# Kernel optimization log

Measured on AMD Instinct MI355X. Metric: run time of the kernel, lower is better.

The kernel has to match this reference:

```python
import jax, jax.numpy as jnp
import numpy as np

DIM = 1024
NUM_HEADS = 16
HEAD_DIM = DIM // NUM_HEADS
B, L = 4, 4096


def setup_inputs() -> dict:
    key = jax.random.key(0)
    ks = jax.random.split(key, 11)
    s = 1.0 / np.sqrt(DIM)
    inp = {
        'q_seq': jax.random.normal(ks[0], (B, L, DIM), jnp.float32),
        'k_seq': jax.random.normal(ks[1], (B, L, DIM), jnp.float32),
        'v_seq': jax.random.normal(ks[2], (B, L, DIM), jnp.float32),
        'Wq': jax.random.normal(ks[3], (DIM, DIM), jnp.float32) * s,
        'bq': jax.random.normal(ks[4], (DIM,), jnp.float32) * s,
        'Wk': jax.random.normal(ks[5], (DIM, DIM), jnp.float32) * s,
        'bk': jax.random.normal(ks[6], (DIM,), jnp.float32) * s,
        'Wv': jax.random.normal(ks[7], (DIM, DIM), jnp.float32) * s,
        'bv': jax.random.normal(ks[8], (DIM,), jnp.float32) * s,
        'Wo': jax.random.normal(ks[9], (DIM, DIM), jnp.float32) * s,
        'bo': jax.random.normal(ks[10], (DIM,), jnp.float32) * s,
        'extract_common': 1,
    }
    return inp


def _heads(x):
    # [B, L, DIM] -> [B, H, L, D]
    Bb, Ll, _ = x.shape
    return x.reshape(Bb, Ll, NUM_HEADS, HEAD_DIM).transpose(0, 2, 1, 3)


def reference(q_seq, k_seq, v_seq, Wq, bq, Wk, bk, Wv, bv, Wo, bo, extract_common):
    Q = _heads(q_seq @ Wq.T + bq)   # [B, H, Lq, D]
    K = _heads(k_seq @ Wk.T + bk)   # [B, H, Lk, D]
    V = _heads(v_seq @ Wv.T + bv)   # [B, H, Lv, D]
    # softmax over the sequence dimension of K (torch dim=2 of [B,H,L,D])
    K_probs = jax.nn.softmax(K, axis=2)
    # context = K_probs^T @ V : [B, H, D, D]
    context = jnp.einsum('bhld,bhle->bhde', K_probs, V)
    attended = jnp.einsum('bhld,bhde->bhle', Q, context)  # [B, H, Lq, D]
    if extract_common:
        target = attended
    else:
        target = V - attended
    Bb, _, Ll, _ = target.shape
    target = target.transpose(0, 2, 1, 3).reshape(Bb, Ll, DIM)
    return target @ Wo.T + bo
```

## Files before the change

kernel.cpp:

```cpp
#include <hip/hip_runtime.h>
#include <cmath>

typedef __bf16 bf16x8 __attribute__((ext_vector_type(8)));
typedef float f32x4 __attribute__((ext_vector_type(4)));
typedef unsigned short us8 __attribute__((ext_vector_type(8)));

__device__ __forceinline__ unsigned short f2bf(float f) {
    union { float f; unsigned u; } x; x.f = f;
    unsigned u = x.u + 0x7FFFu + ((x.u >> 16) & 1u);
    return (unsigned short)(u >> 16);
}
__device__ __forceinline__ float bf2f(unsigned short h) {
    union { unsigned u; float f; } x; x.u = ((unsigned)h) << 16;
    return x.f;
}

__device__ __forceinline__ us8 cvt8(const float* p) {
    f32x4 a = *(const f32x4*)p;
    f32x4 b = *(const f32x4*)(p + 4);
    union { bf16x8 h; us8 u; } cv;
    cv.h[0] = (__bf16)a[0]; cv.h[1] = (__bf16)a[1];
    cv.h[2] = (__bf16)a[2]; cv.h[3] = (__bf16)a[3];
    cv.h[4] = (__bf16)b[0]; cv.h[5] = (__bf16)b[1];
    cv.h[6] = (__bf16)b[2]; cv.h[7] = (__bf16)b[3];
    return cv.u;
}

__device__ __forceinline__ void gl2lds16(const unsigned short* g, unsigned short* l) {
    __builtin_amdgcn_global_load_lds(
        (const __attribute__((address_space(1))) unsigned int*)g,
        (__attribute__((address_space(3))) unsigned int*)l, 16, 0, 0);
}

__global__ __launch_bounds__(256)
void cvt_kernel(const float* __restrict__ src, unsigned short* __restrict__ dst) {
    const size_t i = ((size_t)blockIdx.x * 256 + threadIdx.x) * 8;
    *(us8*)(dst + i) = cvt8(src + i);
}

__global__ __launch_bounds__(256)
void cvt_w4(const float* __restrict__ s0, const float* __restrict__ s1,
            const float* __restrict__ s2, const float* __restrict__ s3,
            unsigned short* __restrict__ d0, unsigned short* __restrict__ d1,
            unsigned short* __restrict__ d2, unsigned short* __restrict__ d3) {
    const float* sp[4] = {s0, s1, s2, s3};
    unsigned short* dp[4] = {d0, d1, d2, d3};
    const float* src = sp[blockIdx.y];
    unsigned short* dst = dp[blockIdx.y];
    const size_t i = ((size_t)blockIdx.x * 256 + threadIdx.x) * 8;
    *(us8*)(dst + i) = cvt8(src + i);
}

__device__ __forceinline__ void swz_tiles(int& m0, int& n0) {
    const int slot = blockIdx.x + (blockIdx.y << 3);
    const int w = ((slot & 7) << 7) | (slot >> 3);
    m0 = (w >> 3) << 7;
    n0 = (w & 7) << 7;
}

template<int MODE, bool BF>
__global__ __launch_bounds__(256)
void gemm_proj(const void* __restrict__ Ap, const void* __restrict__ Wp,
               const float* __restrict__ bias,
               unsigned short* __restrict__ outT,
               float* __restrict__ S)
{
    __shared__ __align__(16) unsigned short lds[17408];

    const int tid = threadIdx.x;
    const int wid = tid >> 6, lane = tid & 63;
    const int quad = lane >> 4, l16 = lane & 15;
    const int waveM = wid >> 1, waveN = wid & 1;
    int m0, n0; swz_tiles(m0, n0);
    const int srow = tid >> 2;
    const int scol = (tid & 3) * 8;
    const int r4 = lane >> 2, c8 = (lane & 3) * 8;

    f32x4 acc[4][4] = {};

    if (BF) {
        const unsigned short* A = (const unsigned short*)Ap;
        const unsigned short* W = (const unsigned short*)Wp;
        for (int s = wid; s < 8; s += 4) {
            const int row = s * 16 + r4;
            gl2lds16(A + (size_t)(m0 + row) * 1024 + c8, lds + s * 512);
            gl2lds16(W + (size_t)(n0 + row) * 1024 + c8, lds + 4096 + s * 512);
        }
    } else {
        const float* A = (const float*)Ap;
        const float* W = (const float*)Wp;
#pragma unroll
        for (int p = 0; p < 2; ++p) {
            const int row = p * 64 + srow;
            *(us8*)(lds + row * 32 + scol) = cvt8(A + (size_t)(m0 + row) * 1024 + scol);
            *(us8*)(lds + 4096 + row * 32 + scol) = cvt8(W + (size_t)(n0 + row) * 1024 + scol);
        }
    }
    __syncthreads();

    int cur = 0;
    for (int k0 = 0; k0 < 1024; k0 += 32) {
        const int nxt = cur ^ 1;
        if (k0 < 992) {
            if (BF) {
                const unsigned short* A = (const unsigned short*)Ap;
                const unsigned short* W = (const unsigned short*)Wp;
                for (int s = wid; s < 8; s += 4) {
                    const int row = s * 16 + r4;
                    gl2lds16(A + (size_t)(m0 + row) * 1024 + k0 + 32 + c8,
                             lds + nxt * 8192 + s * 512);
                    gl2lds16(W + (size_t)(n0 + row) * 1024 + k0 + 32 + c8,
                             lds + nxt * 8192 + 4096 + s * 512);
                }
            } else {
                const float* A = (const float*)Ap;
                const float* W = (const float*)Wp;
#pragma unroll
                for (int p = 0; p < 2; ++p) {
                    const int row = p * 64 + srow;
                    *(us8*)(lds + nxt * 8192 + row * 32 + scol) =
                        cvt8(A + (size_t)(m0 + row) * 1024 + k0 + 32 + scol);
                    *(us8*)(lds + nxt * 8192 + 4096 + row * 32 + scol) =
                        cvt8(W + (size_t)(n0 + row) * 1024 + k0 + 32 + scol);
                }
            }
        }
        const unsigned short* ldsA = lds + cur * 8192;
        const unsigned short* ldsB = ldsA + 4096;
        bf16x8 af[4], bfr[4];
#pragma unroll
        for (int i = 0; i < 4; ++i)
            af[i] = *(const bf16x8*)(ldsA + (waveM * 64 + i * 16 + l16) * 32 + quad * 8);
#pragma unroll
        for (int j = 0; j < 4; ++j)
            bfr[j] = *(const bf16x8*)(ldsB + (waveN * 64 + j * 16 + l16) * 32 + quad * 8);
#pragma unroll
        for (int i = 0; i < 4; ++i)
#pragma unroll
            for (int j = 0; j < 4; ++j)
                acc[i][j] = __builtin_amdgcn_mfma_f32_16x16x32_bf16(af[i], bfr[j], acc[i][j], 0, 0, 0);
        __syncthreads();
        cur = nxt;
    }

    const int b = m0 >> 12, l0 = m0 & 4095;
#pragma unroll
    for (int j = 0; j < 4; ++j) {
        const int nn = waveN * 64 + j * 16 + l16;
        const float bc = bias[n0 + nn];
        float ssum = 0.f;
#pragma unroll
        for (int i = 0; i < 4; ++i)
#pragma unroll
            for (int r = 0; r < 4; ++r) {
                const int mm = waveM * 64 + i * 16 + quad * 4 + r;
                float v = acc[i][j][r] + bc;
                if (MODE == 1) v = expf(fminf(fmaxf(v, -30.f), 30.f));
                lds[nn * 136 + mm] = f2bf(v);
                ssum += v;
            }
        if (MODE == 1) {
            ssum += __shfl_xor(ssum, 16);
            ssum += __shfl_xor(ssum, 32);
            if (lane < 16)
                atomicAdd(&S[(size_t)b * 1024 + n0 + waveN * 64 + j * 16 + lane], ssum);
        }
    }
    __syncthreads();
    const int seg = (tid & 15) * 8;
#pragma unroll
    for (int it = 0; it < 8; ++it) {
        const int nn = (tid >> 4) + it * 16;
        us8 v = *(const us8*)&lds[nn * 136 + seg];
        *(us8*)(outT + ((size_t)b * 1024 + n0 + nn) * 4096 + l0 + seg) = v;
    }
}

__global__ __launch_bounds__(256)
void ctx_kernel(const unsigned short* __restrict__ Vt,
                const unsigned short* __restrict__ Et,
                float* __restrict__ ctxf)
{
    __shared__ __align__(16) unsigned short lds[8192];

    const int tid = threadIdx.x;
    const int wid = tid >> 6, lane = tid & 63;
    const int quad = lane >> 4, l16 = lane & 15;
    const int b = blockIdx.z, h = blockIdx.y;
    const int lbase = blockIdx.x * 512;

    const unsigned short* Arow = Vt + ((size_t)b * 1024 + h * 64) * 4096;
    const unsigned short* Brow = Et + ((size_t)b * 1024 + h * 64) * 4096;

    const int srow = tid >> 2;
    const int scol = (tid & 3) * 8;

    f32x4 acc[4] = {};

    {
        us8 va = *(const us8*)(Arow + (size_t)srow * 4096 + lbase + scol);
        us8 vb = *(const us8*)(Brow + (size_t)srow * 4096 + lbase + scol);
        *(us8*)(lds + srow * 32 + scol) = va;
        *(us8*)(lds + 2048 + srow * 32 + scol) = vb;
    }
    __syncthreads();

    int cur = 0;
    for (int k0 = 0; k0 < 512; k0 += 32) {
        const int nxt = cur ^ 1;
        us8 na = {}, nb = {};
        const bool pf = (k0 < 480);
        if (pf) {
            na = *(const us8*)(Arow + (size_t)srow * 4096 + lbase + k0 + 32 + scol);
            nb = *(const us8*)(Brow + (size_t)srow * 4096 + lbase + k0 + 32 + scol);
        }
        const unsigned short* ldsA = lds + cur * 4096;
        const unsigned short* ldsB = ldsA + 2048;
        bf16x8 a = *(const bf16x8*)(ldsA + (wid * 16 + l16) * 32 + quad * 8);
#pragma unroll
        for (int j = 0; j < 4; ++j) {
            bf16x8 bb = *(const bf16x8*)(ldsB + (j * 16 + l16) * 32 + quad * 8);
            acc[j] = __builtin_amdgcn_mfma_f32_16x16x32_bf16(a, bb, acc[j], 0, 0, 0);
        }
        if (pf) {
            *(us8*)(lds + nxt * 4096 + srow * 32 + scol) = na;
            *(us8*)(lds + nxt * 4096 + 2048 + srow * 32 + scol) = nb;
        }
        __syncthreads();
        cur = nxt;
    }
    float* base = ctxf + ((size_t)(b * 16 + h)) * 4096;
#pragma unroll
    for (int j = 0; j < 4; ++j)
#pragma unroll
        for (int r = 0; r < 4; ++r) {
            const int e = wid * 16 + quad * 4 + r;
            const int d = j * 16 + l16;
            atomicAdd(base + e * 64 + d, acc[j][r]);
        }
}

__global__ __launch_bounds__(256)
void ctx_norm(const float* __restrict__ ctxf, const float* __restrict__ S,
              unsigned short* __restrict__ ctxb)
{
    const int i = blockIdx.x * 256 + threadIdx.x;
    const int d = i & 63;
    const int bh = i >> 12;
    const int b = bh >> 4, h = bh & 15;
    ctxb[i] = f2bf(ctxf[i] / S[b * 1024 + h * 64 + d]);
}

template<bool BF>
__global__ __launch_bounds__(256)
void gemm_qattn(const void* __restrict__ Ap, const void* __restrict__ Wp,
                const float* __restrict__ bias,
                const unsigned short* __restrict__ ctxb,
                const unsigned short* __restrict__ Vt,
                const int* __restrict__ ec,
                unsigned short* __restrict__ att)
{
    __shared__ __align__(16) unsigned short lds[26624];
    unsigned short* ldsQ = lds;
    unsigned short* ldsC = lds + 17408;

    const int tid = threadIdx.x;
    const int wid = tid >> 6, lane = tid & 63;
    const int quad = lane >> 4, l16 = lane & 15;
    const int waveM = wid >> 1, waveN = wid & 1;
    int m0, n0; swz_tiles(m0, n0);
    const int b = m0 >> 12;
    const int srow = tid >> 2, scol = (tid & 3) * 8;
    const int r4 = lane >> 2, c8 = (lane & 3) * 8;

    {
        const int e2 = tid >> 1;
        const int sg = (tid & 1) * 32;
        const unsigned short* src = ctxb +
            (((size_t)(b * 16) + (n0 >> 6) + (e2 >> 6)) * 64 + (e2 & 63)) * 64 + sg;
#pragma unroll
        for (int u = 0; u < 4; ++u)
            *(us8*)&ldsC[e2 * 72 + sg + u * 8] = *(const us8*)(src + u * 8);
    }

    f32x4 acc[4][4] = {};

    if (BF) {
        const unsigned short* A = (const unsigned short*)Ap;
        const unsigned short* W = (const unsigned short*)Wp;
        for (int s = wid; s < 8; s += 4) {
            const int row = s * 16 + r4;
            gl2lds16(A + (size_t)(m0 + row) * 1024 + c8, lds + s * 512);
            gl2lds16(W + (size_t)(n0 + row) * 1024 + c8, lds + 4096 + s * 512);
        }
    } else {
        const float* A = (const float*)Ap;
        const float* W = (const float*)Wp;
#pragma unroll
        for (int p = 0; p < 2; ++p) {
            const int row = p * 64 + srow;
            *(us8*)(lds + row * 32 + scol) = cvt8(A + (size_t)(m0 + row) * 1024 + scol);
            *(us8*)(lds + 4096 + row * 32 + scol) = cvt8(W + (size_t)(n0 + row) * 1024 + scol);
        }
    }
    __syncthreads();

    int cur = 0;
    for (int k0 = 0; k0 < 1024; k0 += 32) {
        const int nxt = cur ^ 1;
        if (k0 < 992) {
            if (BF) {
                const unsigned short* A = (const unsigned short*)Ap;
                const unsigned short* W = (const unsigned short*)Wp;
                for (int s = wid; s < 8; s += 4) {
                    const int row = s * 16 + r4;
                    gl2lds16(A + (size_t)(m0 + row) * 1024 + k0 + 32 + c8,
                             lds + nxt * 8192 + s * 512);
                    gl2lds16(W + (size_t)(n0 + row) * 1024 + k0 + 32 + c8,
                             lds + nxt * 8192 + 4096 + s * 512);
                }
            } else {
                const float* A = (const float*)Ap;
                const float* W = (const float*)Wp;
#pragma unroll
                for (int p = 0; p < 2; ++p) {
                    const int row = p * 64 + srow;
                    *(us8*)(lds + nxt * 8192 + row * 32 + scol) =
                        cvt8(A + (size_t)(m0 + row) * 1024 + k0 + 32 + scol);
                    *(us8*)(lds + nxt * 8192 + 4096 + row * 32 + scol) =
                        cvt8(W + (size_t)(n0 + row) * 1024 + k0 + 32 + scol);
                }
            }
        }
        const unsigned short* ldsA = lds + cur * 8192;
        const unsigned short* ldsB = ldsA + 4096;
        bf16x8 af[4], bfr[4];
#pragma unroll
        for (int i = 0; i < 4; ++i)
            af[i] = *(const bf16x8*)(ldsA + (waveM * 64 + i * 16 + l16) * 32 + quad * 8);
#pragma unroll
        for (int j = 0; j < 4; ++j)
            bfr[j] = *(const bf16x8*)(ldsB + (waveN * 64 + j * 16 + l16) * 32 + quad * 8);
#pragma unroll
        for (int i = 0; i < 4; ++i)
#pragma unroll
            for (int j = 0; j < 4; ++j)
                acc[i][j] = __builtin_amdgcn_mfma_f32_16x16x32_bf16(af[i], bfr[j], acc[i][j], 0, 0, 0);
        __syncthreads();
        cur = nxt;
    }

#pragma unroll
    for (int j = 0; j < 4; ++j) {
        const int nn = waveN * 64 + j * 16 + l16;
        const float bc = bias[n0 + nn];
#pragma unroll
        for (int i = 0; i < 4; ++i)
#pragma unroll
            for (int r = 0; r < 4; ++r) {
                const int mm = waveM * 64 + i * 16 + quad * 4 + r;
                ldsQ[mm * 136 + nn] = f2bf(acc[i][j][r] + bc);
            }
    }
    __syncthreads();

    f32x4 acc2[4][4] = {};
#pragma unroll
    for (int ks = 0; ks < 64; ks += 32) {
        bf16x8 aq[4], cq[4];
#pragma unroll
        for (int i = 0; i < 4; ++i)
            aq[i] = *(const bf16x8*)&ldsQ[(waveM * 64 + i * 16 + l16) * 136 + waveN * 64 + ks + quad * 8];
#pragma unroll
        for (int j = 0; j < 4; ++j)
            cq[j] = *(const bf16x8*)&ldsC[(waveN * 64 + j * 16 + l16) * 72 + ks + quad * 8];
#pragma unroll
        for (int i = 0; i < 4; ++i)
#pragma unroll
            for (int j = 0; j < 4; ++j)
                acc2[i][j] = __builtin_amdgcn_mfma_f32_16x16x32_bf16(aq[i], cq[j], acc2[i][j], 0, 0, 0);
    }

    const int common = ec[0];
#pragma unroll
    for (int i = 0; i < 4; ++i)
#pragma unroll
        for (int j = 0; j < 4; ++j)
#pragma unroll
            for (int r = 0; r < 4; ++r) {
                const int lrow = m0 + waveM * 64 + i * 16 + quad * 4 + r;
                const int chan = n0 + waveN * 64 + j * 16 + l16;
                float vv = acc2[i][j][r];
                if (!common)
                    vv = bf2f(Vt[((size_t)(lrow >> 12) * 1024 + chan) * 4096 + (lrow & 4095)]) - vv;
                att[(size_t)lrow * 1024 + chan] = f2bf(vv);
            }
}

template<bool BF>
__global__ __launch_bounds__(256)
void gemm_out(const unsigned short* __restrict__ A, const void* __restrict__ Wp,
              const float* __restrict__ bias,
              float* __restrict__ outP)
{
    __shared__ __align__(16) unsigned short lds[16384];

    const int tid = threadIdx.x;
    const int wid = tid >> 6, lane = tid & 63;
    const int quad = lane >> 4, l16 = lane & 15;
    const int waveM = wid >> 1, waveN = wid & 1;
    int m0, n0; swz_tiles(m0, n0);
    const int srow = tid >> 2, scol = (tid & 3) * 8;
    const int r4 = lane >> 2, c8 = (lane & 3) * 8;

    f32x4 acc[4][4] = {};

    if (BF) {
        const unsigned short* W = (const unsigned short*)Wp;
        for (int s = wid; s < 8; s += 4) {
            const int row = s * 16 + r4;
            gl2lds16(A + (size_t)(m0 + row) * 1024 + c8, lds + s * 512);
            gl2lds16(W + (size_t)(n0 + row) * 1024 + c8, lds + 4096 + s * 512);
        }
    } else {
        const float* W = (const float*)Wp;
#pragma unroll
        for (int p = 0; p < 2; ++p) {
            const int row = p * 64 + srow;
            *(us8*)(lds + row * 32 + scol) = *(const us8*)(A + (size_t)(m0 + row) * 1024 + scol);
            *(us8*)(lds + 4096 + row * 32 + scol) = cvt8(W + (size_t)(n0 + row) * 1024 + scol);
        }
    }
    __syncthreads();

    int cur = 0;
    for (int k0 = 0; k0 < 1024; k0 += 32) {
        const int nxt = cur ^ 1;
        if (k0 < 992) {
            if (BF) {
                const unsigned short* W = (const unsigned short*)Wp;
                for (int s = wid; s < 8; s += 4) {
                    const int row = s * 16 + r4;
                    gl2lds16(A + (size_t)(m0 + row) * 1024 + k0 + 32 + c8,
                             lds + nxt * 8192 + s * 512);
                    gl2lds16(W + (size_t)(n0 + row) * 1024 + k0 + 32 + c8,
                             lds + nxt * 8192 + 4096 + s * 512);
                }
            } else {
                const float* W = (const float*)Wp;
#pragma unroll
                for (int p = 0; p < 2; ++p) {
                    const int row = p * 64 + srow;
                    *(us8*)(lds + nxt * 8192 + row * 32 + scol) =
                        *(const us8*)(A + (size_t)(m0 + row) * 1024 + k0 + 32 + scol);
                    *(us8*)(lds + nxt * 8192 + 4096 + row * 32 + scol) =
                        cvt8(W + (size_t)(n0 + row) * 1024 + k0 + 32 + scol);
                }
            }
        }
        const unsigned short* ldsA = lds + cur * 8192;
        const unsigned short* ldsB = ldsA + 4096;
        bf16x8 af[4], bfr[4];
#pragma unroll
        for (int i = 0; i < 4; ++i)
            af[i] = *(const bf16x8*)(ldsA + (waveM * 64 + i * 16 + l16) * 32 + quad * 8);
#pragma unroll
        for (int j = 0; j < 4; ++j)
            bfr[j] = *(const bf16x8*)(ldsB + (waveN * 64 + j * 16 + l16) * 32 + quad * 8);
#pragma unroll
        for (int i = 0; i < 4; ++i)
#pragma unroll
            for (int j = 0; j < 4; ++j)
                acc[i][j] = __builtin_amdgcn_mfma_f32_16x16x32_bf16(af[i], bfr[j], acc[i][j], 0, 0, 0);
        __syncthreads();
        cur = nxt;
    }

#pragma unroll
    for (int j = 0; j < 4; ++j) {
        const int col = n0 + waveN * 64 + j * 16 + l16;
        const float bc = bias[col];
#pragma unroll
        for (int i = 0; i < 4; ++i)
#pragma unroll
            for (int r = 0; r < 4; ++r) {
                const int row = m0 + waveM * 64 + i * 16 + quad * 4 + r;
                outP[(size_t)row * 1024 + col] = acc[i][j][r] + bc;
            }
    }
}

extern "C" void kernel_launch(void* const* d_in, const int* in_sizes, int n_in,
                              void* d_out, int out_size, void* d_ws, size_t ws_size,
                              hipStream_t stream)
{
    const float* q  = (const float*)d_in[0];
    const float* k  = (const float*)d_in[1];
    const float* v  = (const float*)d_in[2];
    const float* Wq = (const float*)d_in[3];
    const float* bq = (const float*)d_in[4];
    const float* Wk = (const float*)d_in[5];
    const float* bk = (const float*)d_in[6];
    const float* Wv = (const float*)d_in[7];
    const float* bv = (const float*)d_in[8];
    const float* Wo = (const float*)d_in[9];
    const float* bo = (const float*)d_in[10];
    const int* ec   = (const int*)d_in[11];

    char* ws = (char*)d_ws;
    const size_t NEED_FAST = 110641152;
    const dim3 gblk(8, 128, 1);
    const dim3 gctx(8, 16, 4);

    if (ws_size >= NEED_FAST) {
        unsigned short* Ab   = (unsigned short*)(ws);
        unsigned short* Et   = (unsigned short*)(ws + 33554432);
        unsigned short* Vt   = (unsigned short*)(ws + 67108864);
        unsigned short* Wkb  = (unsigned short*)(ws + 100663296);
        unsigned short* Wvb  = (unsigned short*)(ws + 102760448);
        unsigned short* Wqb  = (unsigned short*)(ws + 104857600);
        unsigned short* Wob  = (unsigned short*)(ws + 106954752);
        float*          ctxf = (float*)(ws + 109051904);
        float*          S    = (float*)(ws + 110100480);
        unsigned short* ctxb = (unsigned short*)(ws + 110116864);
        unsigned short* att  = Et;

        hipMemsetAsync(S, 0, 4096 * sizeof(float), stream);
        hipMemsetAsync(ctxf, 0, 4 * 16 * 64 * 64 * sizeof(float), stream);

        cvt_w4<<<dim3(512, 4), 256, 0, stream>>>(Wk, Wv, Wq, Wo, Wkb, Wvb, Wqb, Wob);

        cvt_kernel<<<8192, 256, 0, stream>>>(k, Ab);
        gemm_proj<1, true><<<gblk, 256, 0, stream>>>(Ab, Wkb, bk, Et, S);

        cvt_kernel<<<8192, 256, 0, stream>>>(v, Ab);
        gemm_proj<2, true><<<gblk, 256, 0, stream>>>(Ab, Wvb, bv, Vt, nullptr);

        ctx_kernel<<<gctx, 256, 0, stream>>>(Vt, Et, ctxf);
        ctx_norm<<<1024, 256, 0, stream>>>(ctxf, S, ctxb);

        cvt_kernel<<<8192, 256, 0, stream>>>(q, Ab);
        gemm_qattn<true><<<gblk, 256, 0, stream>>>(Ab, Wqb, bq, ctxb, Vt, ec, att);

        gemm_out<true><<<gblk, 256, 0, stream>>>(att, Wob, bo, (float*)d_out);
    } else {
        unsigned short* Et   = (unsigned short*)(ws);
        unsigned short* Vt   = (unsigned short*)(ws + 33554432);
        float*          ctxf = (float*)(ws + 67108864);
        float*          S    = (float*)(ws + 68157440);
        unsigned short* ctxb = (unsigned short*)(ws + 68173824);
        unsigned short* att  = Et;

        hipMemsetAsync(S, 0, 4096 * sizeof(float), stream);
        hipMemsetAsync(ctxf, 0, 4 * 16 * 64 * 64 * sizeof(float), stream);

        gemm_proj<1, false><<<gblk, 256, 0, stream>>>(k, Wk, bk, Et, S);
        gemm_proj<2, false><<<gblk, 256, 0, stream>>>(v, Wv, bv, Vt, nullptr);
        ctx_kernel<<<gctx, 256, 0, stream>>>(Vt, Et, ctxf);
        ctx_norm<<<1024, 256, 0, stream>>>(ctxf, S, ctxb);
        gemm_qattn<false><<<gblk, 256, 0, stream>>>(q, Wq, bq, ctxb, Vt, ec, att);
        gemm_out<false><<<gblk, 256, 0, stream>>>(att, Wo, bo, (float*)d_out);
    }
}
```

Before: 458.3 us.

## Triple-buffer async LDS loads in bf16 GEMMs and fuse context normalization into qattn

In the bf16 fast path, the projection, query-attention and output GEMMs now use a three-stage LDS ring filled by direct global-to-LDS loads issued two K-steps ahead. Each step waits with an explicit vmcnt count and a barrier instead of a full __syncthreads. This aims to hide global load latency behind the MFMA work. Separately, the ctx_norm kernel is removed and the division by S is folded into gemm_qattn's load of the context tile, saving one launch and a round trip through memory. The cost is more LDS per block, which may lower occupancy, and the hand-written waitcnt logic must track exactly the number of outstanding loads.

```diff
diff --git a/kernel.cpp b/kernel.cpp
--- a/kernel.cpp
+++ b/kernel.cpp
@@ -15,15 +15,19 @@
     return x.f;
 }
 
-__device__ __forceinline__ us8 cvt8(const float* p) {
-    f32x4 a = *(const f32x4*)p;
-    f32x4 b = *(const f32x4*)(p + 4);
+__device__ __forceinline__ us8 pack8(f32x4 a, f32x4 b) {
     union { bf16x8 h; us8 u; } cv;
     cv.h[0] = (__bf16)a[0]; cv.h[1] = (__bf16)a[1];
     cv.h[2] = (__bf16)a[2]; cv.h[3] = (__bf16)a[3];
     cv.h[4] = (__bf16)b[0]; cv.h[5] = (__bf16)b[1];
     cv.h[6] = (__bf16)b[2]; cv.h[7] = (__bf16)b[3];
     return cv.u;
+}
+
+__device__ __forceinline__ us8 cvt8(const float* p) {
+    f32x4 a = *(const f32x4*)p;
+    f32x4 b = *(const f32x4*)(p + 4);
+    return pack8(a, b);
 }
 
 __device__ __forceinline__ void gl2lds16(const unsigned short* g, unsigned short* l) {
@@ -65,15 +69,14 @@
                unsigned short* __restrict__ outT,
                float* __restrict__ S)
 {
-    __shared__ __align__(16) unsigned short lds[17408];
+    __shared__ __align__(16) unsigned short lds[24576];
 
     const int tid = threadIdx.x;
     const int wid = tid >> 6, lane = tid & 63;
     const int quad = lane >> 4, l16 = lane & 15;
     const int waveM = wid >> 1, waveN = wid & 1;
     int m0, n0; swz_tiles(m0, n0);
-    const int srow = tid >> 2;
-    const int scol = (tid & 3) * 8;
+    const int srow = tid >> 2, scol = (tid & 3) * 8;
     const int r4 = lane >> 2, c8 = (lane & 3) * 8;
 
     f32x4 acc[4][4] = {};
@@ -81,67 +84,87 @@
     if (BF) {
         const unsigned short* A = (const unsigned short*)Ap;
         const unsigned short* W = (const unsigned short*)Wp;
-        for (int s = wid; s < 8; s += 4) {
-            const int row = s * 16 + r4;
-            gl2lds16(A + (size_t)(m0 + row) * 1024 + c8, lds + s * 512);
-            gl2lds16(W + (size_t)(n0 + row) * 1024 + c8, lds + 4096 + s * 512);
-        }
+#define STAGE_P(K0, BASE)                                                     \
+        for (int s = wid; s < 8; s += 4) {                                    \
+            const int row = s * 16 + r4;                                      \
+            gl2lds16(A + (size_t)(m0 + row) * 1024 + (K0) + c8, (BASE) + s * 512);          \
+            gl2lds16(W + (size_t)(n0 + row) * 1024 + (K0) + c8, (BASE) + 4096 + s * 512);   \
+        }
+        STAGE_P(0, lds);
+        STAGE_P(32, lds + 8192);
+        asm volatile("s_waitcnt vmcnt(4) lgkmcnt(0)" ::: "memory");
+        __builtin_amdgcn_s_barrier();
+
+        int cur = 0;
+        for (int it = 0; it < 32; ++it) {
+            if (it < 30) {
+                const int st = (cur >= 1) ? cur - 1 : 2;
+                STAGE_P((it + 2) * 32, lds + st * 8192);
+            }
+            const unsigned short* ldsA = lds + cur * 8192;
+            const unsigned short* ldsB = ldsA + 4096;
+            bf16x8 af[4], bfr[4];
+#pragma unroll
+            for (int i = 0; i < 4; ++i)
+                af[i] = *(const bf16x8*)(ldsA + (waveM * 64 + i * 16 + l16) * 32 + quad * 8);
+#pragma unroll
+            for (int j = 0; j < 4; ++j)
+                bfr[j] = *(const bf16x8*)(ldsB + (waveN * 64 + j * 16 + l16) * 32 + quad * 8);
+#pragma unroll
+            for (int i = 0; i < 4; ++i)
+#pragma unroll
+                for (int j = 0; j < 4; ++j)
+                    acc[i][j] = __builtin_amdgcn_mfma_f32_16x16x32_bf16(af[i], bfr[j], acc[i][j], 0, 0, 0);
+            if (it < 30) {
+                asm volatile("s_waitcnt vmcnt(4) lgkmcnt(0)" ::: "memory");
+                __builtin_amdgcn_s_barrier();
+            } else if (it == 30) {
+                asm volatile("s_waitcnt vmcnt(0) lgkmcnt(0)" ::: "memory");
+                __builtin_amdgcn_s_barrier();
+            }
+            cur = (cur < 2) ? cur + 1 : 0;
+        }
+#undef STAGE_P
     } else {
         const float* A = (const float*)Ap;
         const float* W = (const float*)Wp;
 #pragma unroll
         for (int p = 0; p < 2; ++p) {
-            const int row = p * 64 + srow;
-            *(us8*)(lds + row * 32 + scol) = cvt8(A + (size_t)(m0 + row) * 1024 + scol);
-            *(us8*)(lds + 4096 + row * 32 + scol) = cvt8(W + (size_t)(n0 + row) * 1024 + scol);
+            *(us8*)(lds + (p * 64 + srow) * 32 + scol) = cvt8(A + (size_t)(m0 + p * 64 + srow) * 1024 + scol);
+            *(us8*)(lds + 4096 + (p * 64 + srow) * 32 + scol) = cvt8(W + (size_t)(n0 + p * 64 + srow) * 1024 + scol);
+        }
+        __syncthreads();
+        int cur = 0;
+        for (int k0 = 0; k0 < 1024; k0 += 32) {
+            const int nxt = cur ^ 1;
+            if (k0 < 992) {
+#pragma unroll
+                for (int p = 0; p < 2; ++p) {
+                    *(us8*)(lds + nxt * 8192 + (p * 64 + srow) * 32 + scol) =
+                        cvt8(A + (size_t)(m0 + p * 64 + srow) * 1024 + k0 + 32 + scol);
+                    *(us8*)(lds + nxt * 8192 + 4096 + (p * 64 + srow) * 32 + scol) =
+                        cvt8(W + (size_t)(n0 + p * 64 + srow) * 1024 + k0 + 32 + scol);
+                }
+            }
+            const unsigned short* ldsA = lds + cur * 8192;
+            const unsigned short* ldsB = ldsA + 4096;
+            bf16x8 af[4], bfr[4];
+#pragma unroll
+            for (int i = 0; i < 4; ++i)
+                af[i] = *(const bf16x8*)(ldsA + (waveM * 64 + i * 16 + l16) * 32 + quad * 8);
+#pragma unroll
+            for (int j = 0; j < 4; ++j)
+                bfr[j] = *(const bf16x8*)(ldsB + (waveN * 64 + j * 16 + l16) * 32 + quad * 8);
+#pragma unroll
+            for (int i = 0; i < 4; ++i)
+#pragma unroll
+                for (int j = 0; j < 4; ++j)
+                    acc[i][j] = __builtin_amdgcn_mfma_f32_16x16x32_bf16(af[i], bfr[j], acc[i][j], 0, 0, 0);
+            __syncthreads();
+            cur = nxt;
         }
     }
     __syncthreads();
-
-    int cur = 0;
-    for (int k0 = 0; k0 < 1024; k0 += 32) {
-        const int nxt = cur ^ 1;
-        if (k0 < 992) {
-            if (BF) {
-                const unsigned short* A = (const unsigned short*)Ap;
-                const unsigned short* W = (const unsigned short*)Wp;
-                for (int s = wid; s < 8; s += 4) {
-                    const int row = s * 16 + r4;
-                    gl2lds16(A + (size_t)(m0 + row) * 1024 + k0 + 32 + c8,
-                             lds + nxt * 8192 + s * 512);
-                    gl2lds16(W + (size_t)(n0 + row) * 1024 + k0 + 32 + c8,
-                             lds + nxt * 8192 + 4096 + s * 512);
-                }
-            } else {
-                const float* A = (const float*)Ap;
-                const float* W = (const float*)Wp;
-#pragma unroll
-                for (int p = 0; p < 2; ++p) {
-                    const int row = p * 64 + srow;
-                    *(us8*)(lds + nxt * 8192 + row * 32 + scol) =
-                        cvt8(A + (size_t)(m0 + row) * 1024 + k0 + 32 + scol);
-                    *(us8*)(lds + nxt * 8192 + 4096 + row * 32 + scol) =
-                        cvt8(W + (size_t)(n0 + row) * 1024 + k0 + 32 + scol);
-                }
-            }
-        }
-        const unsigned short* ldsA = lds + cur * 8192;
-        const unsigned short* ldsB = ldsA + 4096;
-        bf16x8 af[4], bfr[4];
-#pragma unroll
-        for (int i = 0; i < 4; ++i)
-            af[i] = *(const bf16x8*)(ldsA + (waveM * 64 + i * 16 + l16) * 32 + quad * 8);
-#pragma unroll
-        for (int j = 0; j < 4; ++j)
-            bfr[j] = *(const bf16x8*)(ldsB + (waveN * 64 + j * 16 + l16) * 32 + quad * 8);
-#pragma unroll
-        for (int i = 0; i < 4; ++i)
-#pragma unroll
-            for (int j = 0; j < 4; ++j)
-                acc[i][j] = __builtin_amdgcn_mfma_f32_16x16x32_bf16(af[i], bfr[j], acc[i][j], 0, 0, 0);
-        __syncthreads();
-        cur = nxt;
-    }
 
     const int b = m0 >> 12, l0 = m0 & 4095;
 #pragma unroll
@@ -240,22 +263,12 @@
         }
 }
 
-__global__ __launch_bounds__(256)
-void ctx_norm(const float* __restrict__ ctxf, const float* __restrict__ S,
-              unsigned short* __restrict__ ctxb)
-{
-    const int i = blockIdx.x * 256 + threadIdx.x;
-    const int d = i & 63;
-    const int bh = i >> 12;
-    const int b = bh >> 4, h = bh & 15;
-    ctxb[i] = f2bf(ctxf[i] / S[b * 1024 + h * 64 + d]);
-}
-
 template<bool BF>
 __global__ __launch_bounds__(256)
 void gemm_qattn(const void* __restrict__ Ap, const void* __restrict__ Wp,
                 const float* __restrict__ bias,
-                const unsigned short* __restrict__ ctxb,
+                const float* __restrict__ ctxf,
+                const float* __restrict__ Sv,
                 const unsigned short* __restrict__ Vt,
                 const int* __restrict__ ec,
                 unsigned short* __restrict__ att)
@@ -273,81 +286,110 @@
     const int srow = tid >> 2, scol = (tid & 3) * 8;
     const int r4 = lane >> 2, c8 = (lane & 3) * 8;
 
+    f32x4 acc[4][4] = {};
+
+    if (BF) {
+        const unsigned short* A = (const unsigned short*)Ap;
+        const unsigned short* W = (const unsigned short*)Wp;
+#define STAGE_Q(K0, BASE)                                                     \
+        for (int s = wid; s < 8; s += 4) {                                    \
+            const int row = s * 16 + r4;                                      \
+            gl2lds16(A + (size_t)(m0 + row) * 1024 + (K0) + c8, (BASE) + s * 512);          \
+            gl2lds16(W + (size_t)(n0 + row) * 1024 + (K0) + c8, (BASE) + 4096 + s * 512);   \
+        }
+        STAGE_Q(0, lds);
+        STAGE_Q(32, lds + 8192);
+        asm volatile("s_waitcnt vmcnt(4) lgkmcnt(0)" ::: "memory");
+        __builtin_amdgcn_s_barrier();
+
+        int cur = 0;
+        for (int it = 0; it < 32; ++it) {
+            if (it < 30) {
+                const int st = (cur >= 1) ? cur - 1 : 2;
+                STAGE_Q((it + 2) * 32, lds + st * 8192);
+            }
+            const unsigned short* ldsA = lds + cur * 8192;
+            const unsigned short* ldsB = ldsA + 4096;
+            bf16x8 af[4], bfr[4];
+#pragma unroll
+            for (int i = 0; i < 4; ++i)
+                af[i] = *(const bf16x8*)(ldsA + (waveM * 64 + i * 16 + l16) * 32 + quad * 8);
+#pragma unroll
+            for (int j = 0; j < 4; ++j)
+                bfr[j] = *(const bf16x8*)(ldsB + (waveN * 64 + j * 16 + l16) * 32 + quad * 8);
+#pragma unroll
+            for (int i = 0; i < 4; ++i)
+#pragma unroll
+                for (int j = 0; j < 4; ++j)
+                    acc[i][j] = __builtin_amdgcn_mfma_f32_16x16x32_bf16(af[i], bfr[j], acc[i][j], 0, 0, 0);
+            if (it < 30) {
+                asm volatile("s_waitcnt vmcnt(4) lgkmcnt(0)" ::: "memory");
+                __builtin_amdgcn_s_barrier();
+            } else if (it == 30) {
+                asm volatile("s_waitcnt vmcnt(0) lgkmcnt(0)" ::: "memory");
+                __builtin_amdgcn_s_barrier();
+            }
+            cur = (cur < 2) ? cur + 1 : 0;
+        }
+#undef STAGE_Q
+    } else {
+        const float* A = (const float*)Ap;
+        const float* W = (const float*)Wp;
+#pragma unroll
+        for (int p = 0; p < 2; ++p) {
+            *(us8*)(lds + (p * 64 + srow) * 32 + scol) = cvt8(A + (size_t)(m0 + p * 64 + srow) * 1024 + scol);
+            *(us8*)(lds + 4096 + (p * 64 + srow) * 32 + scol) = cvt8(W + (size_t)(n0 + p * 64 + srow) * 1024 + scol);
+        }
+        __syncthreads();
+        int cur = 0;
+        for (int k0 = 0; k0 < 1024; k0 += 32) {
+            const int nxt = cur ^ 1;
+            if (k0 < 992) {
+#pragma unroll
+                for (int p = 0; p < 2; ++p) {
+                    *(us8*)(lds + nxt * 8192 + (p * 64 + srow) * 32 + scol) =
+                        cvt8(A + (size_t)(m0 + p * 64 + srow) * 1024 + k0 + 32 + scol);
+                    *(us8*)(lds + nxt * 8192 + 4096 + (p * 64 + srow) * 32 + scol) =
+                        cvt8(W + (size_t)(n0 + p * 64 + srow) * 1024 + k0 + 32 + scol);
+                }
+            }
+            const unsigned short* ldsA = lds + cur * 8192;
+            const unsigned short* ldsB = ldsA + 4096;
+            bf16x8 af[4], bfr[4];
+#pragma unroll
+            for (int i = 0; i < 4; ++i)
+                af[i] = *(const bf16x8*)(ldsA + (waveM * 64 + i * 16 + l16) * 32 + quad * 8);
+#pragma unroll
+            for (int j = 0; j < 4; ++j)
+                bfr[j] = *(const bf16x8*)(ldsB + (waveN * 64 + j * 16 + l16) * 32 + quad * 8);
+#pragma unroll
+            for (int i = 0; i < 4; ++i)
+#pragma unroll
+                for (int j = 0; j < 4; ++j)
+                    acc[i][j] = __builtin_amdgcn_mfma_f32_16x16x32_bf16(af[i], bfr[j], acc[i][j], 0, 0, 0);
+            __syncthreads();
+            cur = nxt;
+        }
+    }
+    __syncthreads();
+
     {
         const int e2 = tid >> 1;
         const int sg = (tid & 1) * 32;
-        const unsigned short* src = ctxb +
-            (((size_t)(b * 16) + (n0 >> 6) + (e2 >> 6)) * 64 + (e2 & 63)) * 64 + sg;
-#pragma unroll
-        for (int u = 0; u < 4; ++u)
-            *(us8*)&ldsC[e2 * 72 + sg + u * 8] = *(const us8*)(src + u * 8);
-    }
-
-    f32x4 acc[4][4] = {};
-
-    if (BF) {
-        const unsigned short* A = (const unsigned short*)Ap;
-        const unsigned short* W = (const unsigned short*)Wp;
-        for (int s = wid; s < 8; s += 4) {
-            const int row = s * 16 + r4;
-            gl2lds16(A + (size_t)(m0 + row) * 1024 + c8, lds + s * 512);
-            gl2lds16(W + (size_t)(n0 + row) * 1024 + c8, lds + 4096 + s * 512);
-        }
-    } else {
-        const float* A = (const float*)Ap;
-        const float* W = (const float*)Wp;
-#pragma unroll
-        for (int p = 0; p < 2; ++p) {
-            const int row = p * 64 + srow;
-            *(us8*)(lds + row * 32 + scol) = cvt8(A + (size_t)(m0 + row) * 1024 + scol);
-            *(us8*)(lds + 4096 + row * 32 + scol) = cvt8(W + (size_t)(n0 + row) * 1024 + scol);
-        }
-    }
-    __syncthreads();
-
-    int cur = 0;
-    for (int k0 = 0; k0 < 1024; k0 += 32) {
-        const int nxt = cur ^ 1;
-        if (k0 < 992) {
-            if (BF) {
-                const unsigned short* A = (const unsigned short*)Ap;
-                const unsigned short* W = (const unsigned short*)Wp;
-                for (int s = wid; s < 8; s += 4) {
-                    const int row = s * 16 + r4;
-                    gl2lds16(A + (size_t)(m0 + row) * 1024 + k0 + 32 + c8,
-                             lds + nxt * 8192 + s * 512);
-                    gl2lds16(W + (size_t)(n0 + row) * 1024 + k0 + 32 + c8,
-                             lds + nxt * 8192 + 4096 + s * 512);
-                }
-            } else {
-                const float* A = (const float*)Ap;
-                const float* W = (const float*)Wp;
-#pragma unroll
-                for (int p = 0; p < 2; ++p) {
-                    const int row = p * 64 + srow;
-                    *(us8*)(lds + nxt * 8192 + row * 32 + scol) =
-                        cvt8(A + (size_t)(m0 + row) * 1024 + k0 + 32 + scol);
-                    *(us8*)(lds + nxt * 8192 + 4096 + row * 32 + scol) =
-                        cvt8(W + (size_t)(n0 + row) * 1024 + k0 + 32 + scol);
-                }
-            }
-        }
-        const unsigned short* ldsA = lds + cur * 8192;
-        const unsigned short* ldsB = ldsA + 4096;
-        bf16x8 af[4], bfr[4];
-#pragma unroll
-        for (int i = 0; i < 4; ++i)
-            af[i] = *(const bf16x8*)(ldsA + (waveM * 64 + i * 16 + l16) * 32 + quad * 8);
-#pragma unroll
-        for (int j = 0; j < 4; ++j)
-            bfr[j] = *(const bf16x8*)(ldsB + (waveN * 64 + j * 16 + l16) * 32 + quad * 8);
-#pragma unroll
-        for (int i = 0; i < 4; ++i)
-#pragma unroll
-            for (int j = 0; j < 4; ++j)
-                acc[i][j] = __builtin_amdgcn_mfma_f32_16x16x32_bf16(af[i], bfr[j], acc[i][j], 0, 0, 0);
-        __syncthreads();
-        cur = nxt;
+        const int hh = (n0 >> 6) + (e2 >> 6);
+        const float* srcf = ctxf + (((size_t)(b * 16) + hh) * 64 + (e2 & 63)) * 64 + sg;
+        const float* Sp = Sv + (size_t)b * 1024 + hh * 64 + sg;
+#pragma unroll
+        for (int u = 0; u < 4; ++u) {
+            f32x4 c0 = *(const f32x4*)(srcf + u * 8);
+            f32x4 c1 = *(const f32x4*)(srcf + u * 8 + 4);
+            union { bf16x8 h; us8 uu; } cv;
+#pragma unroll
+            for (int j = 0; j < 4; ++j) cv.h[j] = (__bf16)(c0[j] / Sp[u * 8 + j]);
+#pragma unroll
+            for (int j = 0; j < 4; ++j) cv.h[4 + j] = (__bf16)(c1[j] / Sp[u * 8 + 4 + j]);
+            *(us8*)&ldsC[(size_t)e2 * 72 + sg + u * 8] = cv.uu;
+        }
     }
 
 #pragma unroll
@@ -403,7 +445,7 @@
               const float* __restrict__ bias,
               float* __restrict__ outP)
 {
-    __shared__ __align__(16) unsigned short lds[16384];
+    __shared__ __align__(16) unsigned short lds[24576];
 
     const int tid = threadIdx.x;
     const int wid = tid >> 6, lane = tid & 63;
@@ -417,63 +459,84 @@
 
     if (BF) {
         const unsigned short* W = (const unsigned short*)Wp;
-        for (int s = wid; s < 8; s += 4) {
-            const int row = s * 16 + r4;
-            gl2lds16(A + (size_t)(m0 + row) * 1024 + c8, lds + s * 512);
-            gl2lds16(W + (size_t)(n0 + row) * 1024 + c8, lds + 4096 + s * 512);
-        }
+#define STAGE_O(K0, BASE)                                                     \
+        for (int s = wid; s < 8; s += 4) {                                    \
+            const int row = s * 16 + r4;                                      \
+            gl2lds16(A + (size_t)(m0 + row) * 1024 + (K0) + c8, (BASE) + s * 512);          \
+            gl2lds16(W + (size_t)(n0 + row) * 1024 + (K0) + c8, (BASE) + 4096 + s * 512);   \
+        }
+        STAGE_O(0, lds);
+        STAGE_O(32, lds + 8192);
+        asm volatile("s_waitcnt vmcnt(4) lgkmcnt(0)" ::: "memory");
+        __builtin_amdgcn_s_barrier();
+
+        int cur = 0;
+        for (int it = 0; it < 32; ++it) {
+            if (it < 30) {
+                const int st = (cur >= 1) ? cur - 1 : 2;
+                STAGE_O((it + 2) * 32, lds + st * 8192);
+            }
+            const unsigned short* ldsA = lds + cur * 8192;
+            const unsigned short* ldsB = ldsA + 4096;
+            bf16x8 af[4], bfr[4];
+#pragma unroll
+            for (int i = 0; i < 4; ++i)
+                af[i] = *(const bf16x8*)(ldsA + (waveM * 64 + i * 16 + l16) * 32 + quad * 8);
+#pragma unroll
+            for (int j = 0; j < 4; ++j)
+                bfr[j] = *(const bf16x8*)(ldsB + (waveN * 64 + j * 16 + l16) * 32 + quad * 8);
+#pragma unroll
+            for (int i = 0; i < 4; ++i)
+#pragma unroll
+                for (int j = 0; j < 4; ++j)
+                    acc[i][j] = __builtin_amdgcn_mfma_f32_16x16x32_bf16(af[i], bfr[j], acc[i][j], 0, 0, 0);
+            if (it < 30) {
+                asm volatile("s_waitcnt vmcnt(4) lgkmcnt(0)" ::: "memory");
+                __builtin_amdgcn_s_barrier();
+            } else if (it == 30) {
+                asm volatile("s_waitcnt vmcnt(0) lgkmcnt(0)" ::: "memory");
+                __builtin_amdgcn_s_barrier();
+            }
+            cur = (cur < 2) ? cur + 1 : 0;
+        }
+#undef STAGE_O
     } else {
         const float* W = (const float*)Wp;
 #pragma unroll
         for (int p = 0; p < 2; ++p) {
-            const int row = p * 64 + srow;
-            *(us8*)(lds + row * 32 + scol) = *(const us8*)(A + (size_t)(m0 + row) * 1024 + scol);
-            *(us8*)(lds + 4096 + row * 32 + scol) = cvt8(W + (size_t)(n0 + row) * 1024 + scol);
-        }
-    }
-    __syncthreads();
-
-    int cur = 0;
-    for (int k0 = 0; k0 < 1024; k0 += 32) {
-        const int nxt = cur ^ 1;
-        if (k0 < 992) {
-            if (BF) {
-                const unsigned short* W = (const unsigned short*)Wp;
-                for (int s = wid; s < 8; s += 4) {
-                    const int row = s * 16 + r4;
-                    gl2lds16(A + (size_t)(m0 + row) * 1024 + k0 + 32 + c8,
-                             lds + nxt * 8192 + s * 512);
-                    gl2lds16(W + (size_t)(n0 + row) * 1024 + k0 + 32 + c8,
-                             lds + nxt * 8192 + 4096 + s * 512);
+            *(us8*)(lds + (p * 64 + srow) * 32 + scol) = *(const us8*)(A + (size_t)(m0 + p * 64 + srow) * 1024 + scol);
+            *(us8*)(lds + 4096 + (p * 64 + srow) * 32 + scol) = cvt8(W + (size_t)(n0 + p * 64 + srow) * 1024 + scol);
+        }
+        __syncthreads();
+        int cur = 0;
+        for (int k0 = 0; k0 < 1024; k0 += 32) {
+            const int nxt = cur ^ 1;
+            if (k0 < 992) {
+#pragma unroll
+                for (int p = 0; p < 2; ++p) {
+                    *(us8*)(lds + nxt * 8192 + (p * 64 + srow) * 32 + scol) =
+                        *(const us8*)(A + (size_t)(m0 + p * 64 + srow) * 1024 + k0 + 32 + scol);
+                    *(us8*)(lds + nxt * 8192 + 4096 + (p * 64 + srow) * 32 + scol) =
+                        cvt8(W + (size_t)(n0 + p * 64 + srow) * 1024 + k0 + 32 + scol);
                 }
-            } else {
-                const float* W = (const float*)Wp;
-#pragma unroll
-                for (int p = 0; p < 2; ++p) {
-                    const int row = p * 64 + srow;
-                    *(us8*)(lds + nxt * 8192 + row * 32 + scol) =
-                        *(const us8*)(A + (size_t)(m0 + row) * 1024 + k0 + 32 + scol);
-                    *(us8*)(lds + nxt * 8192 + 4096 + row * 32 + scol) =
-                        cvt8(W + (size_t)(n0 + row) * 1024 + k0 + 32 + scol);
-                }
-            }
-        }
-        const unsigned short* ldsA = lds + cur * 8192;
-        const unsigned short* ldsB = ldsA + 4096;
-        bf16x8 af[4], bfr[4];
-#pragma unroll
-        for (int i = 0; i < 4; ++i)
-            af[i] = *(const bf16x8*)(ldsA + (waveM * 64 + i * 16 + l16) * 32 + quad * 8);
-#pragma unroll
-        for (int j = 0; j < 4; ++j)
-            bfr[j] = *(const bf16x8*)(ldsB + (waveN * 64 + j * 16 + l16) * 32 + quad * 8);
-#pragma unroll
-        for (int i = 0; i < 4; ++i)
+            }
+            const unsigned short* ldsA = lds + cur * 8192;
+            const unsigned short* ldsB = ldsA + 4096;
+            bf16x8 af[4], bfr[4];
+#pragma unroll
+            for (int i = 0; i < 4; ++i)
+                af[i] = *(const bf16x8*)(ldsA + (waveM * 64 + i * 16 + l16) * 32 + quad * 8);
 #pragma unroll
             for (int j = 0; j < 4; ++j)
-                acc[i][j] = __builtin_amdgcn_mfma_f32_16x16x32_bf16(af[i], bfr[j], acc[i][j], 0, 0, 0);
-        __syncthreads();
-        cur = nxt;
+                bfr[j] = *(const bf16x8*)(ldsB + (waveN * 64 + j * 16 + l16) * 32 + quad * 8);
+#pragma unroll
+            for (int i = 0; i < 4; ++i)
+#pragma unroll
+                for (int j = 0; j < 4; ++j)
+                    acc[i][j] = __builtin_amdgcn_mfma_f32_16x16x32_bf16(af[i], bfr[j], acc[i][j], 0, 0, 0);
+            __syncthreads();
+            cur = nxt;
+        }
     }
 
 #pragma unroll
@@ -522,7 +585,6 @@
         unsigned short* Wob  = (unsigned short*)(ws + 106954752);
         float*          ctxf = (float*)(ws + 109051904);
         float*          S    = (float*)(ws + 110100480);
-        unsigned short* ctxb = (unsigned short*)(ws + 110116864);
         unsigned short* att  = Et;
 
         hipMemsetAsync(S, 0, 4096 * sizeof(float), stream);
@@ -537,10 +599,9 @@
         gemm_proj<2, true><<<gblk, 256, 0, stream>>>(Ab, Wvb, bv, Vt, nullptr);
 
         ctx_kernel<<<gctx, 256, 0, stream>>>(Vt, Et, ctxf);
-        ctx_norm<<<1024, 256, 0, stream>>>(ctxf, S, ctxb);
 
         cvt_kernel<<<8192, 256, 0, stream>>>(q, Ab);
-        gemm_qattn<true><<<gblk, 256, 0, stream>>>(Ab, Wqb, bq, ctxb, Vt, ec, att);
+        gemm_qattn<true><<<gblk, 256, 0, stream>>>(Ab, Wqb, bq, ctxf, S, Vt, ec, att);
 
         gemm_out<true><<<gblk, 256, 0, stream>>>(att, Wob, bo, (float*)d_out);
     } else {
@@ -548,7 +609,6 @@
         unsigned short* Vt   = (unsigned short*)(ws + 33554432);
         float*          ctxf = (float*)(ws + 67108864);
         float*          S    = (float*)(ws + 68157440);
-        unsigned short* ctxb = (unsigned short*)(ws + 68173824);
         unsigned short* att  = Et;
 
         hipMemsetAsync(S, 0, 4096 * sizeof(float), stream);
@@ -557,8 +617,7 @@
         gemm_proj<1, false><<<gblk, 256, 0, stream>>>(k, Wk, bk, Et, S);
         gemm_proj<2, false><<<gblk, 256, 0, stream>>>(v, Wv, bv, Vt, nullptr);
         ctx_kernel<<<gctx, 256, 0, stream>>>(Vt, Et, ctxf);
-        ctx_norm<<<1024, 256, 0, stream>>>(ctxf, S, ctxb);
-        gemm_qattn<false><<<gblk, 256, 0, stream>>>(q, Wq, bq, ctxb, Vt, ec, att);
+        gemm_qattn<false><<<gblk, 256, 0, stream>>>(q, Wq, bq, ctxf, S, Vt, ec, att);
         gemm_out<false><<<gblk, 256, 0, stream>>>(att, Wo, bo, (float*)d_out);
     }
 }
```

Result: no change. 449.3 us (-1.9%).
